# Performance work log

Measured on AMD Instinct MI355X. Metric: run time of the kernel, lower is better.

Reference implementation:

```python
import jax, jax.numpy as jnp
import numpy as np

PI = 3.141592653
MAXV = 8          # max vertices of the intersection of two convex quads
N_BOXES = 1024
IOU_THR = 0.1


def limit_period(val):
    return val - jnp.floor(val / (2.0 * PI) + 0.5) * (2.0 * PI)


def cross2(a, b):
    return a[..., 0] * b[..., 1] - a[..., 1] * b[..., 0]


def rect_corners(box):
    # box: [7] = x,y,z,dx,dy,dz,yaw -> [4,2] BEV corners, CCW order
    x, y, dx, dy, ang = box[0], box[1], box[3], box[4], box[6]
    local = jnp.array([[0.5, 0.5], [-0.5, 0.5], [-0.5, -0.5], [0.5, -0.5]],
                      dtype=box.dtype) * jnp.stack([dx, dy])
    c, s = jnp.cos(ang), jnp.sin(ang)
    rot = jnp.array([[c, -s], [s, c]])
    return local @ rot.T + jnp.stack([x, y])


def poly_area(verts, n):
    # shoelace over first n vertices of padded [MAXV,2] polygon
    idx = jnp.arange(MAXV)
    nxt = verts[jnp.where(idx == n - 1, 0, idx + 1)]
    valid = idx < n
    return 0.5 * jnp.abs(jnp.sum(jnp.where(valid, cross2(verts, nxt), 0.0)))


def bev_inter_area(box_a, box_b):
    # Sutherland-Hodgman: clip quad A against the 4 half-planes of quad B.
    pa = rect_corners(box_a)
    pb = rect_corners(box_b)
    verts0 = jnp.zeros((MAXV, 2), pa.dtype).at[:4].set(pa)
    edges = jnp.stack([pb, jnp.roll(pb, -1, axis=0)], axis=1)  # [4,2,2]

    def clip(carry, e):
        v, n = carry
        a, b = e[0], e[1]
        idx = jnp.arange(MAXV)
        prev = v[jnp.where(idx == 0, n - 1, idx - 1)]
        d = b - a
        sp = cross2(d, v - a)     # signed side of current vertex
        sq = cross2(d, prev - a)  # signed side of previous vertex
        in_p, in_q = sp >= 0, sq >= 0
        den = sq - sp
        den = jnp.where(jnp.abs(den) < 1e-9, 1e-9, den)
        t = sq / den
        inter = prev + t[:, None] * (v - prev)
        live = idx < n
        emit_i = live & (in_p != in_q)   # crossing -> emit intersection
        emit_p = live & in_p             # inside -> emit vertex
        pts = jnp.stack([inter, v], axis=1).reshape(2 * MAXV, 2)
        msk = jnp.stack([emit_i, emit_p], axis=1).reshape(2 * MAXV)
        pos = jnp.where(msk, jnp.cumsum(msk) - 1, MAXV)  # compact; OOB dropped
        nv = jnp.zeros((MAXV, 2), v.dtype).at[pos].set(pts, mode='drop')
        return (nv, jnp.sum(msk).astype(jnp.int32)), None

    (v, n), _ = jax.lax.scan(clip, (verts0, jnp.int32(4)), edges)
    return jnp.where(n >= 3, poly_area(v, n), 0.0)


def iou3d_pair(a, b):
    inter_bev = bev_inter_area(a, b)
    h = jnp.maximum(jnp.minimum(a[2] + a[5] * 0.5, b[2] + b[5] * 0.5)
                    - jnp.maximum(a[2] - a[5] * 0.5, b[2] - b[5] * 0.5), 0.0)
    inter = inter_bev * h
    va = a[3] * a[4] * a[5]
    vb = b[3] * b[4] * b[5]
    return inter / jnp.maximum(va + vb - inter, 1e-6)


def clustering(ious):
    # exact translation of the sequential while-loop: repeatedly take the
    # first unassigned box, assign everything with iou > 0.1 to a new cluster
    # id (later clusters may overwrite earlier assignments, as in the source).
    N = ious.shape[0]

    def body(i, carry):
        ci, cid = carry
        has_zero = jnp.any(ci == 0)
        cur = jnp.argmax(ci == 0)
        m = ious[cur] > IOU_THR
        ci = jnp.where(has_zero & m, cid, ci)
        return (ci, cid + has_zero.astype(jnp.int32))

    ci, _ = jax.lax.fori_loop(0, N, body, (jnp.zeros(N, jnp.int32), jnp.int32(1)))
    return ci


def fuse_cluster(m, boxes, scores):
    # m: bool[N] membership mask for one cluster
    s = jnp.where(m, scores, 0.0)
    ssum = jnp.sum(s)
    dirs = boxes[:, 6]
    ref = dirs[jnp.argmax(s)]                    # direction of max-score member
    diff = jnp.abs(dirs - ref)
    diff = jnp.where(diff > PI, 2.0 * PI - diff, diff)
    gt = diff > PI / 2
    sc_gt = jnp.sum(jnp.where(m & gt, scores, 0.0))
    sc_le = ssum - sc_gt
    flip_gt = sc_gt <= sc_le                     # flip minority orientation group
    add = jnp.where(flip_gt, gt, ~gt)
    d2 = limit_period(dirs + PI * add.astype(boxes.dtype))
    sn = s / jnp.where(ssum > 0, ssum, 1.0)
    theta = jnp.arctan2(jnp.sum(jnp.sin(d2) * sn), jnp.sum(jnp.cos(d2) * sn))
    center = jnp.sum(boxes[:, :6] * sn[:, None], axis=0)
    box_f = jnp.concatenate([center, theta[None]])
    # score fusion: sum_i s_(i)^(i+1) over descending-sorted member scores
    s_sorted = jnp.sort(s)[::-1]
    powers = jnp.arange(1, s.shape[0] + 1, dtype=s.dtype)
    s_f = jnp.minimum(jnp.sum(s_sorted ** powers), 1.0)
    return box_f, s_f


def setup_inputs() -> dict:
    key = jax.random.key(0)
    k = jax.random.split(key, 6)
    xy = jax.random.uniform(k[0], (N_BOXES, 2), minval=0.0, maxval=140.0)
    z = jax.random.uniform(k[1], (N_BOXES, 1), minval=-1.0, maxval=1.0)
    dxy = jax.random.uniform(k[2], (N_BOXES, 2), minval=1.5, maxval=4.5)
    dz = jax.random.uniform(k[3], (N_BOXES, 1), minval=1.0, maxval=2.0)
    yaw = jax.random.uniform(k[4], (N_BOXES, 1), minval=-PI, maxval=PI)
    det_boxes = jnp.concatenate([xy, z, dxy, dz, yaw], axis=1)
    det_scores = jax.random.uniform(k[5], (N_BOXES,), minval=0.01, maxval=1.0)
    return {"det_boxes": det_boxes, "det_scores": det_scores}


def reference(det_boxes, det_scores):
    N = det_boxes.shape[0]
    boxes = det_boxes.at[:, 6].set(limit_period(det_boxes[:, 6]))
    ious = jax.vmap(lambda a: jax.vmap(lambda b: iou3d_pair(a, b))(boxes))(boxes)
    ci = clustering(ious)                               # int32[N], ids in 1..N
    masks = ci[None, :] == jnp.arange(1, N + 1)[:, None]  # [N clusters, N boxes]
    boxes_f, scores_f = jax.vmap(fuse_cluster, in_axes=(0, None, None))(masks, boxes, det_scores)
    valid = jnp.any(masks, axis=1)
    boxes_f = jnp.where(valid[:, None], boxes_f, 0.0)
    scores_f = jnp.where(valid, scores_f, 0.0)
    return boxes_f, scores_f, valid
```

## Files before the change

### kernel.cpp

```cpp
#include <hip/hip_runtime.h>

#define PI_F 3.141592653f
#define NB 1024
#define NW 16
#define IOU_THR_F 0.1f

__device__ __forceinline__ float limit_period_f(float v) {
    return v - floorf(v / (2.0f * PI_F) + 0.5f) * (2.0f * PI_F);
}

__device__ __forceinline__ int widx(int r, int w) {
    return (r << 4) | (w ^ (r & 15));
}

__global__ __launch_bounds__(256) void iouT_kernel(
    const float* __restrict__ boxes,
    unsigned long long* __restrict__ maskT,
    unsigned char* __restrict__ flagT)
{
    __shared__ float vxs[2][8][256];
    __shared__ float vys[2][8][256];
    const int tid = threadIdx.x;
    const int j = blockIdx.x;

    const float xj  = boxes[j*7+0], yj  = boxes[j*7+1], zj  = boxes[j*7+2];
    const float dxj = boxes[j*7+3], dyj = boxes[j*7+4], dzj = boxes[j*7+5];
    const float bang = limit_period_f(boxes[j*7+6]);
    const float rb2 = 0.25f*(dxj*dxj + dyj*dyj);
    float cb, sb;
    sincosf(bang, &sb, &cb);

    float pbx[4], pby[4];
    {
        const float hx = 0.5f*dxj, hy = 0.5f*dyj;
        const float lxs[4] = { hx, -hx, -hx, hx };
        const float lys[4] = { hy, hy, -hy, -hy };
        #pragma unroll
        for (int k = 0; k < 4; ++k) {
            pbx[k] = lxs[k]*cb - lys[k]*sb + xj;
            pby[k] = lxs[k]*sb + lys[k]*cb + yj;
        }
    }
    const float vb = dxj*dyj*dzj;

    #pragma unroll
    for (int q = 0; q < 4; ++q) {
        const int i = q*256 + tid;
        const float xi  = boxes[i*7+0], yi  = boxes[i*7+1];
        const float dxi = boxes[i*7+3], dyi = boxes[i*7+4];
        const float ddx = xi - xj, ddy = yi - yj;
        const float d2 = ddx*ddx + ddy*ddy;
        const float ra2 = 0.25f*(dxi*dxi + dyi*dyi);
        const bool cand = d2 <= 2.0f*(ra2 + rb2);

        bool bit = false;
        if (__ballot(cand) != 0ull) {
            if (cand) {
                const float zi  = boxes[i*7+2], dzi = boxes[i*7+5];
                const float aang = limit_period_f(boxes[i*7+6]);
                float ca, sa;
                sincosf(aang, &sa, &ca);
                {
                    const float hx = 0.5f*dxi, hy = 0.5f*dyi;
                    const float lxs[4] = { hx, -hx, -hx, hx };
                    const float lys[4] = { hy, hy, -hy, -hy };
                    #pragma unroll
                    for (int k = 0; k < 4; ++k) {
                        vxs[0][k][tid] = lxs[k]*ca - lys[k]*sa + xi;
                        vys[0][k][tid] = lxs[k]*sa + lys[k]*ca + yi;
                    }
                }

                int n = 4;
                int cur = 0;
                #pragma unroll
                for (int e = 0; e < 4; ++e) {
                    const float eax = pbx[e], eay = pby[e];
                    const float ebx2 = pbx[(e+1)&3], eby2 = pby[(e+1)&3];
                    const float dx = ebx2 - eax, dy = eby2 - eay;
                    int m = 0;
                    if (n > 0) {
                        int pidx = n - 1; if (pidx > 7) pidx = 7;
                        float px = vxs[cur][pidx][tid];
                        float py = vys[cur][pidx][tid];
                        float sq = dx*(py - eay) - dy*(px - eax);
                        #pragma unroll
                        for (int k = 0; k < 8; ++k) {
                            if (k < n) {
                                const float cx = vxs[cur][k][tid];
                                const float cy = vys[cur][k][tid];
                                const float sp = dx*(cy - eay) - dy*(cx - eax);
                                const bool in_p = (sp >= 0.0f);
                                const bool in_q = (sq >= 0.0f);
                                if (in_p != in_q) {
                                    float den = sq - sp;
                                    den = (fabsf(den) < 1e-9f) ? 1e-9f : den;
                                    const float t = sq / den;
                                    if (m < 8) {
                                        vxs[cur^1][m][tid] = px + t*(cx - px);
                                        vys[cur^1][m][tid] = py + t*(cy - py);
                                    }
                                    ++m;
                                }
                                if (in_p) {
                                    if (m < 8) {
                                        vxs[cur^1][m][tid] = cx;
                                        vys[cur^1][m][tid] = cy;
                                    }
                                    ++m;
                                }
                                px = cx; py = cy; sq = sp;
                            }
                        }
                    }
                    n = m;
                    cur ^= 1;
                }

                float area = 0.0f;
                if (n >= 3) {
                    float s = 0.0f;
                    const float x0 = vxs[cur][0][tid];
                    const float y0 = vys[cur][0][tid];
                    #pragma unroll
                    for (int k = 0; k < 8; ++k) {
                        if (k < n) {
                            float nx, ny;
                            if (k == n - 1) { nx = x0; ny = y0; }
                            else {
                                int nk = k + 1; if (nk > 7) nk = 7;
                                nx = vxs[cur][nk][tid]; ny = vys[cur][nk][tid];
                            }
                            s += vxs[cur][k][tid]*ny - vys[cur][k][tid]*nx;
                        }
                    }
                    area = 0.5f * fabsf(s);
                }

                const float zh = fminf(zi + dzi*0.5f, zj + dzj*0.5f);
                const float zl = fmaxf(zi - dzi*0.5f, zj - dzj*0.5f);
                const float h = fmaxf(zh - zl, 0.0f);
                const float inter = area * h;
                const float va = dxi*dyi*dzi;
                const float iou = inter / fmaxf(va + vb - inter, 1e-6f);
                bit = iou > IOU_THR_F;
            }
        }

        const unsigned long long bal = __ballot(bit);
        if ((tid & 63) == 0) {
            const int w = q*4 + (tid >> 6);
            maskT[(size_t)j*NW + w] = bal;
            flagT[j*NW + w] = (bal != 0ull) ? 1 : 0;
        }
    }
}

__global__ __launch_bounds__(256) void cluster_kernel(
    const unsigned long long* __restrict__ maskT,
    const unsigned char* __restrict__ flagT,
    int* __restrict__ ci_out)
{
    extern __shared__ char smem[];
    unsigned long long* mat = (unsigned long long*)smem;
    unsigned short* wm = (unsigned short*)(smem + 131072);
    unsigned long long* seed_lds = (unsigned long long*)(smem + 133120);
    int* rankb = (int*)(smem + 133248);

    const int tid = threadIdx.x;

    if (tid < NW) { seed_lds[tid] = 0ull; rankb[tid] = 0; }
    #pragma unroll
    for (int rr = 0; rr < 4; ++rr) {
        const int r = tid + rr * 256;
        const uint4 f = *(const uint4*)(flagT + r * NW);
        unsigned int m16 = 0;
        #define NIBX(v, sh) \
            { if ((v) & 0x000000FFu) m16 |= 1u << (sh); \
              if ((v) & 0x0000FF00u) m16 |= 1u << ((sh)+1); \
              if ((v) & 0x00FF0000u) m16 |= 1u << ((sh)+2); \
              if ((v) & 0xFF000000u) m16 |= 1u << ((sh)+3); }
        NIBX(f.x, 0) NIBX(f.y, 4) NIBX(f.z, 8) NIBX(f.w, 12)
        #undef NIBX
        wm[r] = (unsigned short)m16;
        unsigned int t16 = m16;
        while (t16) {
            const int w = __ffs(t16) - 1;
            t16 &= t16 - 1;
            mat[widx(r, w)] = maskT[r * NW + w];
        }
    }
    __syncthreads();

    if (tid < 64) {
        int base = 0;
        for (int c = 0; c < NW; ++c) {
            const int row = c * 64 + tid;
            unsigned int f = (unsigned int)wm[row];
            unsigned long long acc = 0ull, Dt = 0ull;
            while (f) {
                const int w = __ffs(f) - 1;
                f &= f - 1;
                const unsigned long long v = mat[widx(row, w)];
                acc |= v & seed_lds[w];
                if (w == c) Dt = v;
            }
            const bool elig = (acc == 0ull);
            const unsigned long long E = __ballot(elig);
            const unsigned long long inlow = Dt & ((1ull << tid) - 1ull);

            unsigned long long S = E;
            #pragma unroll 1
            for (int it = 0; it < 64; ++it) {
                const bool killed = (inlow & S) != 0ull;
                const unsigned long long S2 = E & __ballot(!killed);
                if (S2 == S) break;
                S = S2;
            }

            if (tid == 0) { seed_lds[c] = S; rankb[c] = base; }
            base += (int)__popcll(S);
        }
    }
    __syncthreads();

    #pragma unroll
    for (int rr = 0; rr < 4; ++rr) {
        const int r = tid + rr * 256;
        unsigned int f = (unsigned int)wm[r];
        int best = -1;
        while (f) {
            const int w = __ffs(f) - 1;
            f &= f - 1;
            const unsigned long long bits = mat[widx(r, w)] & seed_lds[w];
            if (bits) best = (w << 6) | (63 - __clzll(bits));
        }
        int lbl = 0;
        if (best >= 0) {
            const int w = best >> 6, pos = best & 63;
            lbl = rankb[w] + (int)__popcll(seed_lds[w] & ((1ull << pos) - 1ull)) + 1;
        }
        ci_out[r] = lbl;
    }
}

__global__ __launch_bounds__(64) void fuse_kernel(
    const float* __restrict__ boxes,
    const float* __restrict__ scores,
    const int* __restrict__ ci,
    float* __restrict__ out)
{
    __shared__ float ms[NB];
    __shared__ int   mi[NB];

    const int b = blockIdx.x;
    const int lane = threadIdx.x;
    const int target = b + 1;

    unsigned int mymask = 0;
    const int4* ci4 = (const int4*)ci;
    #pragma unroll
    for (int k4 = 0; k4 < 4; ++k4) {
        const int4 v = ci4[lane * 4 + k4];
        if (v.x == target) mymask |= 1u << (k4*4+0);
        if (v.y == target) mymask |= 1u << (k4*4+1);
        if (v.z == target) mymask |= 1u << (k4*4+2);
        if (v.w == target) mymask |= 1u << (k4*4+3);
    }
    const bool anyv = (__ballot(mymask != 0) != 0ULL);

    float* outb = out + (size_t)b * 7;
    float* outs = out + 7 * NB;
    float* outv = out + 8 * NB;

    if (!anyv) {
        if (lane == 0) {
            #pragma unroll
            for (int c = 0; c < 7; ++c) outb[c] = 0.0f;
            outs[b] = 0.0f;
            outv[b] = 0.0f;
        }
        return;
    }

    float ssum = 0.0f, smax = -1.0f;
    int sidx = 1 << 30;
    #pragma unroll
    for (int k = 0; k < 16; ++k) {
        if (mymask & (1u << k)) {
            const int idx = lane * 16 + k;
            const float s = scores[idx];
            ssum += s;
            if (s > smax || (s == smax && idx < sidx)) { smax = s; sidx = idx; }
        }
    }
    #pragma unroll
    for (int off = 32; off >= 1; off >>= 1) {
        ssum += __shfl_xor(ssum, off);
        const float om = __shfl_xor(smax, off);
        const int   oi = __shfl_xor(sidx, off);
        if (om > smax || (om == smax && oi < sidx)) { smax = om; sidx = oi; }
    }
    const float ref = limit_period_f(boxes[sidx * 7 + 6]);

    float sc_gt = 0.0f;
    #pragma unroll
    for (int k = 0; k < 16; ++k) {
        if (mymask & (1u << k)) {
            const int idx = lane * 16 + k;
            const float dir = limit_period_f(boxes[idx * 7 + 6]);
            float diff = fabsf(dir - ref);
            if (diff > PI_F) diff = 2.0f * PI_F - diff;
            if (diff > PI_F * 0.5f) sc_gt += scores[idx];
        }
    }
    #pragma unroll
    for (int off = 32; off >= 1; off >>= 1) sc_gt += __shfl_xor(sc_gt, off);
    const bool flip_gt = (sc_gt <= (ssum - sc_gt));

    float acc[6] = {0,0,0,0,0,0};
    float ssin = 0.0f, scos = 0.0f;
    #pragma unroll
    for (int k = 0; k < 16; ++k) {
        if (mymask & (1u << k)) {
            const int idx = lane * 16 + k;
            const float s = scores[idx];
            const float w = s / ssum;
            const float dir = limit_period_f(boxes[idx * 7 + 6]);
            float diff = fabsf(dir - ref);
            if (diff > PI_F) diff = 2.0f * PI_F - diff;
            const bool gt = (diff > PI_F * 0.5f);
            const bool add = flip_gt ? gt : (!gt);
            const float d2 = limit_period_f(dir + (add ? PI_F : 0.0f));
            float sd, cd;
            sincosf(d2, &sd, &cd);
            ssin += sd * w;
            scos += cd * w;
            #pragma unroll
            for (int c = 0; c < 6; ++c) acc[c] += boxes[idx * 7 + c] * w;
        }
    }
    #pragma unroll
    for (int off = 32; off >= 1; off >>= 1) {
        ssin += __shfl_xor(ssin, off);
        scos += __shfl_xor(scos, off);
        #pragma unroll
        for (int c = 0; c < 6; ++c) acc[c] += __shfl_xor(acc[c], off);
    }
    const float theta = atan2f(ssin, scos);

    const int cnt = __popc(mymask);
    int x = cnt;
    #pragma unroll
    for (int off = 1; off < 64; off <<= 1) {
        const int y = __shfl_up(x, off);
        if (lane >= off) x += y;
    }
    const int base = x - cnt;
    const int K = __shfl(x, 63);
    {
        int p = base;
        #pragma unroll
        for (int k = 0; k < 16; ++k) {
            if (mymask & (1u << k)) {
                const int idx = lane * 16 + k;
                ms[p] = scores[idx];
                mi[p] = idx;
                ++p;
            }
        }
    }
    __syncthreads();

    float sf = 0.0f;
    for (int e = lane; e < K; e += 64) {
        const float v = ms[e];
        const int ix = mi[e];
        int rank = 0;
        for (int t = 0; t < K; ++t) {
            const float u = ms[t];
            if (u > v || (u == v && mi[t] < ix)) ++rank;
        }
        sf += powf(v, (float)(rank + 1));
    }
    #pragma unroll
    for (int off = 32; off >= 1; off >>= 1) sf += __shfl_xor(sf, off);
    sf = fminf(sf, 1.0f);

    if (lane == 0) {
        #pragma unroll
        for (int c = 0; c < 6; ++c) outb[c] = acc[c];
        outb[6] = theta;
        outs[b] = sf;
        outv[b] = 1.0f;
    }
}

extern "C" void kernel_launch(void* const* d_in, const int* in_sizes, int n_in,
                              void* d_out, int out_size, void* d_ws, size_t ws_size,
                              hipStream_t stream) {
    const float* boxes  = (const float*)d_in[0];
    const float* scores = (const float*)d_in[1];
    float* out = (float*)d_out;

    unsigned long long* maskT = (unsigned long long*)d_ws;
    int* ci = (int*)((char*)d_ws + 131072);
    unsigned char* flagT = (unsigned char*)d_ws + 135168;

    iouT_kernel<<<NB, 256, 0, stream>>>(boxes, maskT, flagT);

    const size_t SMEM = 133312;
    (void)hipFuncSetAttribute((const void*)cluster_kernel,
                              hipFuncAttributeMaxDynamicSharedMemorySize, (int)SMEM);
    cluster_kernel<<<1, 256, SMEM, stream>>>(maskT, flagT, ci);

    fuse_kernel<<<NB, 64, 0, stream>>>(boxes, scores, ci, out);
}
```

Baseline: 91.06 us.

## Compact candidate pairs into a list before the exact IoU pass

Splits the IoU kernel into a cheap prefilter and an exact pass. The prefilter writes candidate ballots into the mask and appends each off-diagonal candidate pair to a global list through a per-wave atomic counter. A second grid-stride kernel runs polygon clipping only on the listed pairs and clears the mask bits that fail the threshold. This removes wave divergence, since only dense, useful work runs the expensive path. It adds a memset, an extra launch, contention on one atomic counter, and flag bytes that can stay set for words later cleared to zero.

```diff
diff --git a/kernel.cpp b/kernel.cpp
--- a/kernel.cpp
+++ b/kernel.cpp
@@ -13,35 +13,20 @@
     return (r << 4) | (w ^ (r & 15));
 }
 
-__global__ __launch_bounds__(256) void iouT_kernel(
+__global__ __launch_bounds__(256) void prefilter_kernel(
     const float* __restrict__ boxes,
     unsigned long long* __restrict__ maskT,
-    unsigned char* __restrict__ flagT)
+    unsigned char* __restrict__ flagT,
+    unsigned int* __restrict__ counter,
+    unsigned int* __restrict__ candlist)
 {
-    __shared__ float vxs[2][8][256];
-    __shared__ float vys[2][8][256];
     const int tid = threadIdx.x;
+    const int lane = tid & 63;
     const int j = blockIdx.x;
 
-    const float xj  = boxes[j*7+0], yj  = boxes[j*7+1], zj  = boxes[j*7+2];
-    const float dxj = boxes[j*7+3], dyj = boxes[j*7+4], dzj = boxes[j*7+5];
-    const float bang = limit_period_f(boxes[j*7+6]);
+    const float xj  = boxes[j*7+0], yj  = boxes[j*7+1];
+    const float dxj = boxes[j*7+3], dyj = boxes[j*7+4];
     const float rb2 = 0.25f*(dxj*dxj + dyj*dyj);
-    float cb, sb;
-    sincosf(bang, &sb, &cb);
-
-    float pbx[4], pby[4];
-    {
-        const float hx = 0.5f*dxj, hy = 0.5f*dyj;
-        const float lxs[4] = { hx, -hx, -hx, hx };
-        const float lys[4] = { hy, hy, -hy, -hy };
-        #pragma unroll
-        for (int k = 0; k < 4; ++k) {
-            pbx[k] = lxs[k]*cb - lys[k]*sb + xj;
-            pby[k] = lxs[k]*sb + lys[k]*cb + yj;
-        }
-    }
-    const float vb = dxj*dyj*dzj;
 
     #pragma unroll
     for (int q = 0; q < 4; ++q) {
@@ -53,105 +38,150 @@
         const float ra2 = 0.25f*(dxi*dxi + dyi*dyi);
         const bool cand = d2 <= 2.0f*(ra2 + rb2);
 
-        bool bit = false;
-        if (__ballot(cand) != 0ull) {
-            if (cand) {
-                const float zi  = boxes[i*7+2], dzi = boxes[i*7+5];
-                const float aang = limit_period_f(boxes[i*7+6]);
-                float ca, sa;
-                sincosf(aang, &sa, &ca);
-                {
-                    const float hx = 0.5f*dxi, hy = 0.5f*dyi;
-                    const float lxs[4] = { hx, -hx, -hx, hx };
-                    const float lys[4] = { hy, hy, -hy, -hy };
-                    #pragma unroll
-                    for (int k = 0; k < 4; ++k) {
-                        vxs[0][k][tid] = lxs[k]*ca - lys[k]*sa + xi;
-                        vys[0][k][tid] = lxs[k]*sa + lys[k]*ca + yi;
+        const unsigned long long bal = __ballot(cand);
+        const int w = q*4 + (tid >> 6);
+        if (lane == 0) {
+            maskT[(size_t)j*NW + w] = bal;
+            flagT[j*NW + w] = (bal != 0ull) ? 1 : 0;
+        }
+
+        unsigned long long keep = bal;
+        if ((j >> 6) == w) keep &= ~(1ull << (j & 63));
+        unsigned int base = 0;
+        if (lane == 0 && keep) base = atomicAdd(counter, (unsigned)__popcll(keep));
+        base = __shfl(base, 0);
+        if ((keep >> lane) & 1ull) {
+            const unsigned int pos = base + (unsigned)__popcll(keep & ((1ull << lane) - 1ull));
+            candlist[pos] = ((unsigned)j << 10) | (unsigned)i;
+        }
+    }
+}
+
+__global__ __launch_bounds__(256) void iou_exact_kernel(
+    const float* __restrict__ boxes,
+    const unsigned int* __restrict__ counter,
+    const unsigned int* __restrict__ candlist,
+    unsigned long long* __restrict__ maskT)
+{
+    __shared__ float vxs[2][8][256];
+    __shared__ float vys[2][8][256];
+    const int tid = threadIdx.x;
+    const unsigned int total = counter[0];
+
+    for (unsigned int idx = blockIdx.x*256 + tid; idx < total; idx += gridDim.x*256) {
+        const unsigned int e = candlist[idx];
+        const int j = (int)(e >> 10);
+        const int i = (int)(e & 1023u);
+
+        const float xi  = boxes[i*7+0], yi  = boxes[i*7+1], zi  = boxes[i*7+2];
+        const float dxi = boxes[i*7+3], dyi = boxes[i*7+4], dzi = boxes[i*7+5];
+        const float aang = limit_period_f(boxes[i*7+6]);
+        const float xj  = boxes[j*7+0], yj  = boxes[j*7+1], zj  = boxes[j*7+2];
+        const float dxj = boxes[j*7+3], dyj = boxes[j*7+4], dzj = boxes[j*7+5];
+        const float bang = limit_period_f(boxes[j*7+6]);
+
+        float ca, sa, cb, sb;
+        sincosf(aang, &sa, &ca);
+        sincosf(bang, &sb, &cb);
+
+        {
+            const float hx = 0.5f*dxi, hy = 0.5f*dyi;
+            const float lxs[4] = { hx, -hx, -hx, hx };
+            const float lys[4] = { hy, hy, -hy, -hy };
+            #pragma unroll
+            for (int k = 0; k < 4; ++k) {
+                vxs[0][k][tid] = lxs[k]*ca - lys[k]*sa + xi;
+                vys[0][k][tid] = lxs[k]*sa + lys[k]*ca + yi;
+            }
+        }
+        float pbx[4], pby[4];
+        {
+            const float hx = 0.5f*dxj, hy = 0.5f*dyj;
+            const float lxs[4] = { hx, -hx, -hx, hx };
+            const float lys[4] = { hy, hy, -hy, -hy };
+            #pragma unroll
+            for (int k = 0; k < 4; ++k) {
+                pbx[k] = lxs[k]*cb - lys[k]*sb + xj;
+                pby[k] = lxs[k]*sb + lys[k]*cb + yj;
+            }
+        }
+
+        int n = 4;
+        int cur = 0;
+        #pragma unroll
+        for (int e4 = 0; e4 < 4; ++e4) {
+            const float eax = pbx[e4], eay = pby[e4];
+            const float ebx2 = pbx[(e4+1)&3], eby2 = pby[(e4+1)&3];
+            const float dx = ebx2 - eax, dy = eby2 - eay;
+            int m = 0;
+            if (n > 0) {
+                int pidx = n - 1; if (pidx > 7) pidx = 7;
+                float px = vxs[cur][pidx][tid];
+                float py = vys[cur][pidx][tid];
+                float sq = dx*(py - eay) - dy*(px - eax);
+                #pragma unroll
+                for (int k = 0; k < 8; ++k) {
+                    if (k < n) {
+                        const float cx = vxs[cur][k][tid];
+                        const float cy = vys[cur][k][tid];
+                        const float sp = dx*(cy - eay) - dy*(cx - eax);
+                        const bool in_p = (sp >= 0.0f);
+                        const bool in_q = (sq >= 0.0f);
+                        if (in_p != in_q) {
+                            float den = sq - sp;
+                            den = (fabsf(den) < 1e-9f) ? 1e-9f : den;
+                            const float t = sq / den;
+                            if (m < 8) {
+                                vxs[cur^1][m][tid] = px + t*(cx - px);
+                                vys[cur^1][m][tid] = py + t*(cy - py);
+                            }
+                            ++m;
+                        }
+                        if (in_p) {
+                            if (m < 8) {
+                                vxs[cur^1][m][tid] = cx;
+                                vys[cur^1][m][tid] = cy;
+                            }
+                            ++m;
+                        }
+                        px = cx; py = cy; sq = sp;
                     }
                 }
-
-                int n = 4;
-                int cur = 0;
-                #pragma unroll
-                for (int e = 0; e < 4; ++e) {
-                    const float eax = pbx[e], eay = pby[e];
-                    const float ebx2 = pbx[(e+1)&3], eby2 = pby[(e+1)&3];
-                    const float dx = ebx2 - eax, dy = eby2 - eay;
-                    int m = 0;
-                    if (n > 0) {
-                        int pidx = n - 1; if (pidx > 7) pidx = 7;
-                        float px = vxs[cur][pidx][tid];
-                        float py = vys[cur][pidx][tid];
-                        float sq = dx*(py - eay) - dy*(px - eax);
-                        #pragma unroll
-                        for (int k = 0; k < 8; ++k) {
-                            if (k < n) {
-                                const float cx = vxs[cur][k][tid];
-                                const float cy = vys[cur][k][tid];
-                                const float sp = dx*(cy - eay) - dy*(cx - eax);
-                                const bool in_p = (sp >= 0.0f);
-                                const bool in_q = (sq >= 0.0f);
-                                if (in_p != in_q) {
-                                    float den = sq - sp;
-                                    den = (fabsf(den) < 1e-9f) ? 1e-9f : den;
-                                    const float t = sq / den;
-                                    if (m < 8) {
-                                        vxs[cur^1][m][tid] = px + t*(cx - px);
-                                        vys[cur^1][m][tid] = py + t*(cy - py);
-                                    }
-                                    ++m;
-                                }
-                                if (in_p) {
-                                    if (m < 8) {
-                                        vxs[cur^1][m][tid] = cx;
-                                        vys[cur^1][m][tid] = cy;
-                                    }
-                                    ++m;
-                                }
-                                px = cx; py = cy; sq = sp;
-                            }
-                        }
+            }
+            n = m;
+            cur ^= 1;
+        }
+
+        float area = 0.0f;
+        if (n >= 3) {
+            float s = 0.0f;
+            const float x0 = vxs[cur][0][tid];
+            const float y0 = vys[cur][0][tid];
+            #pragma unroll
+            for (int k = 0; k < 8; ++k) {
+                if (k < n) {
+                    float nx, ny;
+                    if (k == n - 1) { nx = x0; ny = y0; }
+                    else {
+                        int nk = k + 1; if (nk > 7) nk = 7;
+                        nx = vxs[cur][nk][tid]; ny = vys[cur][nk][tid];
                     }
-                    n = m;
-                    cur ^= 1;
+                    s += vxs[cur][k][tid]*ny - vys[cur][k][tid]*nx;
                 }
-
-                float area = 0.0f;
-                if (n >= 3) {
-                    float s = 0.0f;
-                    const float x0 = vxs[cur][0][tid];
-                    const float y0 = vys[cur][0][tid];
-                    #pragma unroll
-                    for (int k = 0; k < 8; ++k) {
-                        if (k < n) {
-                            float nx, ny;
-                            if (k == n - 1) { nx = x0; ny = y0; }
-                            else {
-                                int nk = k + 1; if (nk > 7) nk = 7;
-                                nx = vxs[cur][nk][tid]; ny = vys[cur][nk][tid];
-                            }
-                            s += vxs[cur][k][tid]*ny - vys[cur][k][tid]*nx;
-                        }
-                    }
-                    area = 0.5f * fabsf(s);
-                }
-
-                const float zh = fminf(zi + dzi*0.5f, zj + dzj*0.5f);
-                const float zl = fmaxf(zi - dzi*0.5f, zj - dzj*0.5f);
-                const float h = fmaxf(zh - zl, 0.0f);
-                const float inter = area * h;
-                const float va = dxi*dyi*dzi;
-                const float iou = inter / fmaxf(va + vb - inter, 1e-6f);
-                bit = iou > IOU_THR_F;
-            }
-        }
-
-        const unsigned long long bal = __ballot(bit);
-        if ((tid & 63) == 0) {
-            const int w = q*4 + (tid >> 6);
-            maskT[(size_t)j*NW + w] = bal;
-            flagT[j*NW + w] = (bal != 0ull) ? 1 : 0;
+            }
+            area = 0.5f * fabsf(s);
+        }
+
+        const float zh = fminf(zi + dzi*0.5f, zj + dzj*0.5f);
+        const float zl = fmaxf(zi - dzi*0.5f, zj - dzj*0.5f);
+        const float h = fmaxf(zh - zl, 0.0f);
+        const float inter = area * h;
+        const float va = dxi*dyi*dzi;
+        const float vb = dxj*dyj*dzj;
+        const float iou = inter / fmaxf(va + vb - inter, 1e-6f);
+
+        if (!(iou > IOU_THR_F)) {
+            atomicAnd(&maskT[(size_t)j*NW + (i >> 6)], ~(1ull << (i & 63)));
         }
     }
 }
@@ -406,8 +436,13 @@
     unsigned long long* maskT = (unsigned long long*)d_ws;
     int* ci = (int*)((char*)d_ws + 131072);
     unsigned char* flagT = (unsigned char*)d_ws + 135168;
-
-    iouT_kernel<<<NB, 256, 0, stream>>>(boxes, maskT, flagT);
+    unsigned int* counter = (unsigned int*)((char*)d_ws + 151552);
+    unsigned int* candlist = (unsigned int*)((char*)d_ws + 151616);
+
+    hipMemsetAsync(counter, 0, sizeof(unsigned int), stream);
+
+    prefilter_kernel<<<NB, 256, 0, stream>>>(boxes, maskT, flagT, counter, candlist);
+    iou_exact_kernel<<<64, 256, 0, stream>>>(boxes, counter, candlist, maskT);
 
     const size_t SMEM = 133312;
     (void)hipFuncSetAttribute((const void*)cluster_kernel,
```

Result: slower. 122.5 us (+34.6%).
